# Kernel tuning notes

Measured on AMD Instinct MI355X. Metric: run time of the kernel, lower is better.

The kernel has to match this reference:

```python
import jax, jax.numpy as jnp
import numpy as np

DIM_Q = 512
DIM_K = 512
DIM_V = 512
NUM_HEADS = 8
TEMPERATURE = 0.1
LN_EPS = 1e-5


def setup_inputs() -> dict:
    key = jax.random.key(0)
    ks = jax.random.split(key, 12)
    B, n_q, n_k = 8, 1024, 1024
    s = 0.02
    return {
        "Q": jax.random.normal(ks[0], (B, n_q, DIM_Q), jnp.float32),
        "K": jax.random.normal(ks[1], (B, n_k, DIM_K), jnp.float32),
        "mask": jnp.ones((B, n_k), dtype=bool),
        "Wq": jax.random.normal(ks[2], (DIM_Q, DIM_V), jnp.float32) * s,
        "bq": jnp.zeros((DIM_V,), jnp.float32),
        "Wk": jax.random.normal(ks[3], (DIM_K, DIM_V), jnp.float32) * s,
        "bk": jnp.zeros((DIM_V,), jnp.float32),
        "Wv": jax.random.normal(ks[4], (DIM_K, DIM_V), jnp.float32) * s,
        "bv": jnp.zeros((DIM_V,), jnp.float32),
        "Wo": jax.random.normal(ks[5], (DIM_V, DIM_V), jnp.float32) * s,
        "bo": jnp.zeros((DIM_V,), jnp.float32),
        "gamma": jnp.ones((DIM_V,), jnp.float32),
        "beta": jnp.zeros((DIM_V,), jnp.float32),
    }


def _mab(Q, K, mask, Wq, bq, Wk, bk, Wv, bv, Wo, bo, gamma, beta):
    B, n_q, _ = Q.shape
    n_k = K.shape[1]
    H = NUM_HEADS
    d_head = DIM_V // H
    # projections, split heads: [B, H, n, d_head]
    Qh = (Q @ Wq + bq).reshape(B, n_q, H, d_head).transpose(0, 2, 1, 3)
    Kh = (K @ Wk + bk).reshape(B, n_k, H, d_head).transpose(0, 2, 1, 3)
    Vh = (K @ Wv + bv).reshape(B, n_k, H, d_head).transpose(0, 2, 1, 3)
    scale = 1.0 / (np.sqrt(d_head) * TEMPERATURE)
    A = jnp.einsum("bhqd,bhkd->bhqk", Qh, Kh) * scale
    A = jnp.where(mask[:, None, None, :], A, -jnp.inf)
    A = jax.nn.softmax(A, axis=-1)
    O = jnp.einsum("bhqk,bhkd->bhqd", A, Vh)
    O = O.transpose(0, 2, 1, 3).reshape(B, n_q, DIM_V)
    # fused output FFN + residual + LN
    O = O + jax.nn.relu(O @ Wo + bo)
    mu = jnp.mean(O, axis=-1, keepdims=True)
    var = jnp.var(O, axis=-1, keepdims=True)
    return (O - mu) * jax.lax.rsqrt(var + LN_EPS) * gamma + beta


def reference(Q, K, mask, Wq, bq, Wk, bk, Wv, bv, Wo, bo, gamma, beta):
    return _mab(Q, K, mask, Wq, bq, Wk, bk, Wv, bv, Wo, bo, gamma, beta)
```

## Files before the change

kernel.cpp:

```cpp
#include <hip/hip_runtime.h>

typedef __bf16 bf16;
typedef bf16 bf16x4 __attribute__((ext_vector_type(4)));
typedef bf16 bf16x8 __attribute__((ext_vector_type(8)));
typedef float floatx4 __attribute__((ext_vector_type(4)));

#define NB 8
#define NQ 1024
#define NK 1024
#define DIM 512
#define NH 8
#define DH 64

__device__ __forceinline__ void async16(const void* g, void* l) {
    __builtin_amdgcn_global_load_lds(
        (const __attribute__((address_space(1))) unsigned int*)(unsigned long long)(g),
        (__attribute__((address_space(3))) unsigned int*)(unsigned long long)(l),
        16, 0, 0);
}

__global__ __launch_bounds__(256) void prep_fused(
    const float* __restrict__ Q, const float* __restrict__ K,
    const float* __restrict__ Wq, const float* __restrict__ Wk,
    const float* __restrict__ Wv, const float* __restrict__ Wo,
    bf16* __restrict__ Qb, bf16* __restrict__ Kb, bf16* __restrict__ Wt)
{
    __shared__ bf16 Tl[64][68];
    const int bid = blockIdx.x;
    if (bid < 4096) {
        const int i = bid * 256 + threadIdx.x;
        float4 a = ((const float4*)Q)[i];
        float4 c = ((const float4*)K)[i];
        bf16x4 qa = {(bf16)a.x, (bf16)a.y, (bf16)a.z, (bf16)a.w};
        bf16x4 ka = {(bf16)c.x, (bf16)c.y, (bf16)c.z, (bf16)c.w};
        *(bf16x4*)(Qb + (size_t)i * 4) = qa;
        *(bf16x4*)(Kb + (size_t)i * 4) = ka;
    } else {
        const int bid2 = bid - 4096;
        const int w = bid2 >> 6;
        const int bx = bid2 & 7, by = (bid2 >> 3) & 7;
        const float* W = (w == 0) ? Wq : (w == 1) ? Wk : (w == 2) ? Wv : Wo;
        bf16* out = Wt + (size_t)w * DIM * DIM;
        const int k0 = bx * 64, n0 = by * 64;
        const int tx = threadIdx.x & 15, ty = threadIdx.x >> 4;
        for (int pass = 0; pass < 4; ++pass) {
            int k = ty + pass * 16;
            float4 v = *(const float4*)&W[(size_t)(k0 + k) * DIM + n0 + tx * 4];
            Tl[tx * 4 + 0][k] = (bf16)v.x;
            Tl[tx * 4 + 1][k] = (bf16)v.y;
            Tl[tx * 4 + 2][k] = (bf16)v.z;
            Tl[tx * 4 + 3][k] = (bf16)v.w;
        }
        __syncthreads();
        for (int pass = 0; pass < 4; ++pass) {
            int n = ty + pass * 16;
            bf16x4 ov = *(const bf16x4*)&Tl[n][tx * 4];
            *(bf16x4*)&out[(size_t)(n0 + n) * DIM + k0 + tx * 4] = ov;
        }
    }
}

__global__ __launch_bounds__(256) void proj_fused(
    const bf16* __restrict__ Qb, const bf16* __restrict__ Kb,
    const bf16* __restrict__ Wt,
    const float* __restrict__ bq, const float* __restrict__ bk,
    const float* __restrict__ bv,
    bf16* __restrict__ Qp, bf16* __restrict__ Kp, bf16* __restrict__ Vpt)
{
    __shared__ __attribute__((aligned(16))) bf16 sh[32768];
    const int t = threadIdx.x;
    const int wave = t >> 6, lane = t & 63, quad = lane >> 4, l16 = lane & 15;
    const int wr = wave >> 1, wc = wave & 1;
    const int bid = blockIdx.x;
    const bool isQ = bid < 256;
    const bf16* A; const bf16* W; int m0, n0;
    if (isQ) { A = Qb; W = Wt;             m0 = (bid & 63) * 128;  n0 = (bid >> 6) * 128; }
    else     { int b2 = bid - 256;
               A = Kb; W = Wt + 512 * DIM; m0 = (b2 & 63) * 128;   n0 = (b2 >> 6) * 128; }

    const int r1 = t >> 3, s1 = t & 7;
    const int p1 = s1 ^ (r1 & 7);
    const bf16* aSrc = A + (size_t)(m0 + r1) * DIM + p1 * 8;
    const bf16* wSrc = W + (size_t)(n0 + r1) * DIM + p1 * 8;

    floatx4 acc[4][4];
    for (int i = 0; i < 4; ++i)
        for (int j = 0; j < 4; ++j) acc[i][j] = (floatx4){0.f, 0.f, 0.f, 0.f};

    #pragma unroll
    for (int j = 0; j < 4; ++j) {
        async16(aSrc + (size_t)j * 32 * DIM, sh + (t + j * 256) * 8);
        async16(wSrc + (size_t)j * 32 * DIM, sh + 16384 + (t + j * 256) * 8);
    }

    for (int kt = 0; kt < 8; ++kt) {
        __syncthreads();
        const int cur = kt & 1;
        bf16* Acur = sh + cur * 8192;
        bf16* Bcur = sh + 16384 + cur * 8192;
        if (kt < 7) {
            bf16* Anxt = sh + (1 - cur) * 8192;
            bf16* Bnxt = sh + 16384 + (1 - cur) * 8192;
            const int ko = (kt + 1) * 64;
            #pragma unroll
            for (int j = 0; j < 4; ++j) {
                async16(aSrc + ko + (size_t)j * 32 * DIM, Anxt + (t + j * 256) * 8);
                async16(wSrc + ko + (size_t)j * 32 * DIM, Bnxt + (t + j * 256) * 8);
            }
        }
        #pragma unroll
        for (int ks = 0; ks < 2; ++ks) {
            bf16x8 af[4], bfr[4];
            #pragma unroll
            for (int mi = 0; mi < 4; ++mi) {
                const int row = wr * 64 + mi * 16 + l16;
                af[mi] = *(const bf16x8*)(Acur + row * 64 + (((ks * 4 + quad) ^ (row & 7)) << 3));
            }
            #pragma unroll
            for (int ni = 0; ni < 4; ++ni) {
                const int row = wc * 64 + ni * 16 + l16;
                bfr[ni] = *(const bf16x8*)(Bcur + row * 64 + (((ks * 4 + quad) ^ (row & 7)) << 3));
            }
            #pragma unroll
            for (int mi = 0; mi < 4; ++mi)
                #pragma unroll
                for (int ni = 0; ni < 4; ++ni)
                    acc[mi][ni] = __builtin_amdgcn_mfma_f32_16x16x32_bf16(
                        af[mi], bfr[ni], acc[mi][ni], 0, 0, 0);
        }
    }

    const bool isV = (!isQ) && (n0 >= 512);
    if (!isV) {
        bf16* out = isQ ? Qp : Kp;
        const float* bias = isQ ? bq : bk;
        for (int ni = 0; ni < 4; ++ni) {
            const int n = n0 + wc * 64 + ni * 16 + l16;
            const float bb = bias[n];
            const int hd = n >> 6, d = n & 63;
            for (int mi = 0; mi < 4; ++mi) {
                for (int r = 0; r < 4; ++r) {
                    const int m = m0 + wr * 64 + mi * 16 + quad * 4 + r;
                    const int b = m >> 10, q = m & 1023;
                    out[((size_t)(b * 8 + hd) * 1024 + q) * 64 + d] = (bf16)(acc[mi][ni][r] + bb);
                }
            }
        }
    } else {
        __syncthreads();
        for (int ni = 0; ni < 4; ++ni) {
            const int n = wc * 64 + ni * 16 + l16;
            const float bb = bv[n0 + n - 512];
            for (int mi = 0; mi < 4; ++mi) {
                const int mb = wr * 64 + mi * 16 + quad * 4;
                const int slot = ((mb >> 3) ^ (n & 15));
                bf16x4 pk = {(bf16)(acc[mi][ni][0] + bb), (bf16)(acc[mi][ni][1] + bb),
                             (bf16)(acc[mi][ni][2] + bb), (bf16)(acc[mi][ni][3] + bb)};
                *(bf16x4*)(sh + n * 128 + slot * 8 + (mb & 7)) = pk;
            }
        }
        __syncthreads();
        const int n = t >> 1, hf = t & 1;
        const int nv = n0 + n - 512, hd = nv >> 6, d = nv & 63;
        const int b = m0 >> 10, qb = m0 & 1023;
        bf16* dst = Vpt + ((size_t)(b * 8 + hd) * 64 + d) * 1024 + qb + hf * 64;
        #pragma unroll
        for (int j = 0; j < 8; ++j) {
            const int ch = hf * 8 + j;
            const int slot = ch ^ (n & 15);
            bf16x8 v8 = *(const bf16x8*)(sh + n * 128 + slot * 8);
            *(bf16x8*)(dst + j * 8) = v8;
        }
    }
}

__global__ __launch_bounds__(256) void attn_kernel(
    const bf16* __restrict__ Qp, const bf16* __restrict__ Kp,
    const bf16* __restrict__ Vpt, const int* __restrict__ mask,
    bf16* __restrict__ Oa)
{
    const int bh = blockIdx.x & 63, qblk = blockIdx.x >> 6;
    const int b = bh >> 3, hd = bh & 7;
    const int t = threadIdx.x;
    const int wave = t >> 6, lane = t & 63, quad = lane >> 4, l16 = lane & 15;
    const float scale = 1.25f;

    __shared__ __attribute__((aligned(16))) bf16 Kt[2][64 * 64];
    __shared__ __attribute__((aligned(16))) bf16 Vt[2][64 * 64];
    __shared__ __attribute__((aligned(16))) bf16 Pl[4][32 * 64];

    const bf16* Qbase = Qp + ((size_t)bh * NQ + qblk * 128 + wave * 32) * DH;
    const bf16* Kbase = Kp + (size_t)bh * NK * DH;
    const bf16* Vbase = Vpt + (size_t)bh * DH * NK;
    const int* mrow = mask + b * NK;

    bf16x8 qf[2][2];
    for (int g = 0; g < 2; ++g)
        for (int hh = 0; hh < 2; ++hh)
            qf[g][hh] = *(const bf16x8*)(Qbase + (g * 16 + l16) * DH + hh * 32 + quad * 8);

    floatx4 o[2][4];
    float lsum[2];
    for (int g = 0; g < 2; ++g) {
        lsum[g] = 0.f;
        for (int i = 0; i < 4; ++i) o[g][i] = (floatx4){0.f, 0.f, 0.f, 0.f};
    }

    const int r1 = t >> 3, s1 = t & 7;
    const int p1 = s1 ^ (r1 & 7);
    const bf16* kSrc = Kbase + r1 * 64 + p1 * 8;
    const bf16* vSrc = Vbase + (size_t)r1 * 1024 + p1 * 8;

    async16(kSrc, Kt[0] + t * 8);
    async16(kSrc + 32 * 64, Kt[0] + (t + 256) * 8);
    async16(vSrc, Vt[0] + t * 8);
    async16(vSrc + (size_t)32 * 1024, Vt[0] + (t + 256) * 8);

    for (int kt = 0; kt < NK / 64; ++kt) {
        __syncthreads();
        const int cur = kt & 1;
        if (kt < NK / 64 - 1) {
            const int nxt = 1 - cur;
            async16(kSrc + (kt + 1) * 4096, Kt[nxt] + t * 8);
            async16(kSrc + (kt + 1) * 4096 + 32 * 64, Kt[nxt] + (t + 256) * 8);
            async16(vSrc + (kt + 1) * 64, Vt[nxt] + t * 8);
            async16(vSrc + (kt + 1) * 64 + (size_t)32 * 1024, Vt[nxt] + (t + 256) * 8);
        }

        bf16x8 kb[4][2];
        #pragma unroll
        for (int sub = 0; sub < 4; ++sub) {
            const int rowk = sub * 16 + l16;
            kb[sub][0] = *(const bf16x8*)(Kt[cur] + rowk * 64 + ((quad ^ (rowk & 7)) << 3));
            kb[sub][1] = *(const bf16x8*)(Kt[cur] + rowk * 64 + (((quad + 4) ^ (rowk & 7)) << 3));
        }
        floatx4 sf[2][4];
        #pragma unroll
        for (int g = 0; g < 2; ++g)
            #pragma unroll
            for (int sub = 0; sub < 4; ++sub) {
                floatx4 s = {0.f, 0.f, 0.f, 0.f};
                s = __builtin_amdgcn_mfma_f32_16x16x32_bf16(kb[sub][0], qf[g][0], s, 0, 0, 0);
                s = __builtin_amdgcn_mfma_f32_16x16x32_bf16(kb[sub][1], qf[g][1], s, 0, 0, 0);
                sf[g][sub] = s;
            }
        #pragma unroll
        for (int sub = 0; sub < 4; ++sub) {
            const int4 m4 = *(const int4*)&mrow[kt * 64 + sub * 16 + quad * 4];
            const float md0 = m4.x ? 0.f : -3.0e38f;
            const float md1 = m4.y ? 0.f : -3.0e38f;
            const float md2 = m4.z ? 0.f : -3.0e38f;
            const float md3 = m4.w ? 0.f : -3.0e38f;
            #pragma unroll
            for (int g = 0; g < 2; ++g) {
                float p0 = __expf(sf[g][sub][0] * scale + md0);
                float p1v = __expf(sf[g][sub][1] * scale + md1);
                float p2 = __expf(sf[g][sub][2] * scale + md2);
                float p3 = __expf(sf[g][sub][3] * scale + md3);
                sf[g][sub][0] = p0; sf[g][sub][1] = p1v;
                sf[g][sub][2] = p2; sf[g][sub][3] = p3;
                lsum[g] += p0 + p1v + p2 + p3;
            }
        }
        #pragma unroll
        for (int g = 0; g < 2; ++g)
            #pragma unroll
            for (int sub = 0; sub < 4; ++sub) {
                bf16x4 pk = {(bf16)sf[g][sub][0], (bf16)sf[g][sub][1],
                             (bf16)sf[g][sub][2], (bf16)sf[g][sub][3]};
                const int slot = (sub * 2 + (quad >> 1)) ^ (l16 & 7);
                *(bf16x4*)&Pl[wave][(g * 16 + l16) * 64 + slot * 8 + (quad & 1) * 4] = pk;
            }
        bf16x8 af[2][2];
        #pragma unroll
        for (int g = 0; g < 2; ++g)
            #pragma unroll
            for (int hh = 0; hh < 2; ++hh) {
                const int slot = (hh * 4 + quad) ^ (l16 & 7);
                af[g][hh] = *(const bf16x8*)&Pl[wave][(g * 16 + l16) * 64 + slot * 8];
            }
        #pragma unroll
        for (int dsub = 0; dsub < 4; ++dsub) {
            const int rowd = dsub * 16 + l16;
            bf16x8 v0 = *(const bf16x8*)(Vt[cur] + rowd * 64 + ((quad ^ (rowd & 7)) << 3));
            bf16x8 v1 = *(const bf16x8*)(Vt[cur] + rowd * 64 + (((quad + 4) ^ (rowd & 7)) << 3));
            #pragma unroll
            for (int g = 0; g < 2; ++g) {
                o[g][dsub] = __builtin_amdgcn_mfma_f32_16x16x32_bf16(af[g][0], v0, o[g][dsub], 0, 0, 0);
                o[g][dsub] = __builtin_amdgcn_mfma_f32_16x16x32_bf16(af[g][1], v1, o[g][dsub], 0, 0, 0);
            }
        }
    }

    for (int g = 0; g < 2; ++g) {
        float lr = lsum[g];
        lr += __shfl_xor(lr, 16, 64);
        lr += __shfl_xor(lr, 32, 64);
        const float inv = 1.f / lr;
        float linv[4];
        for (int r = 0; r < 4; ++r) linv[r] = __shfl(inv, quad * 4 + r, 64);
        for (int dsub = 0; dsub < 4; ++dsub) {
            for (int r = 0; r < 4; ++r) {
                const int q = qblk * 128 + wave * 32 + g * 16 + quad * 4 + r;
                const int col = hd * 64 + dsub * 16 + l16;
                Oa[((size_t)(b * NQ + q)) * DIM + col] = (bf16)(o[g][dsub][r] * linv[r]);
            }
        }
    }
}

__global__ __launch_bounds__(256) void ffn_gemm(
    const bf16* __restrict__ Oa, const bf16* __restrict__ W,
    const float* __restrict__ bias, bf16* __restrict__ Yb)
{
    __shared__ __attribute__((aligned(16))) bf16 sh[32768];
    const int t = threadIdx.x;
    const int wave = t >> 6, lane = t & 63, quad = lane >> 4, l16 = lane & 15;
    const int wr = wave >> 1, wc = wave & 1;
    const int m0 = (blockIdx.x & 63) * 128, n0 = (blockIdx.x >> 6) * 128;

    const int r1 = t >> 3, s1 = t & 7;
    const int p1 = s1 ^ (r1 & 7);
    const bf16* aSrc = Oa + (size_t)(m0 + r1) * DIM + p1 * 8;
    const bf16* wSrc = W  + (size_t)(n0 + r1) * DIM + p1 * 8;

    floatx4 acc[4][4];
    for (int i = 0; i < 4; ++i)
        for (int j = 0; j < 4; ++j) acc[i][j] = (floatx4){0.f, 0.f, 0.f, 0.f};

    #pragma unroll
    for (int j = 0; j < 4; ++j) {
        async16(aSrc + (size_t)j * 32 * DIM, sh + (t + j * 256) * 8);
        async16(wSrc + (size_t)j * 32 * DIM, sh + 16384 + (t + j * 256) * 8);
    }

    for (int kt = 0; kt < 8; ++kt) {
        __syncthreads();
        const int cur = kt & 1;
        bf16* Acur = sh + cur * 8192;
        bf16* Bcur = sh + 16384 + cur * 8192;
        if (kt < 7) {
            bf16* Anxt = sh + (1 - cur) * 8192;
            bf16* Bnxt = sh + 16384 + (1 - cur) * 8192;
            const int ko = (kt + 1) * 64;
            #pragma unroll
            for (int j = 0; j < 4; ++j) {
                async16(aSrc + ko + (size_t)j * 32 * DIM, Anxt + (t + j * 256) * 8);
                async16(wSrc + ko + (size_t)j * 32 * DIM, Bnxt + (t + j * 256) * 8);
            }
        }
        #pragma unroll
        for (int ks = 0; ks < 2; ++ks) {
            bf16x8 af[4], bfr[4];
            #pragma unroll
            for (int mi = 0; mi < 4; ++mi) {
                const int row = wr * 64 + mi * 16 + l16;
                af[mi] = *(const bf16x8*)(Acur + row * 64 + (((ks * 4 + quad) ^ (row & 7)) << 3));
            }
            #pragma unroll
            for (int ni = 0; ni < 4; ++ni) {
                const int row = wc * 64 + ni * 16 + l16;
                bfr[ni] = *(const bf16x8*)(Bcur + row * 64 + (((ks * 4 + quad) ^ (row & 7)) << 3));
            }
            #pragma unroll
            for (int mi = 0; mi < 4; ++mi)
                #pragma unroll
                for (int ni = 0; ni < 4; ++ni)
                    acc[mi][ni] = __builtin_amdgcn_mfma_f32_16x16x32_bf16(
                        af[mi], bfr[ni], acc[mi][ni], 0, 0, 0);
        }
    }

    for (int ni = 0; ni < 4; ++ni) {
        const int n = n0 + wc * 64 + ni * 16 + l16;
        const float bb = bias[n];
        for (int mi = 0; mi < 4; ++mi) {
            for (int r = 0; r < 4; ++r) {
                const int m = m0 + wr * 64 + mi * 16 + quad * 4 + r;
                const float ov = (float)Oa[(size_t)m * DIM + n];
                Yb[(size_t)m * DIM + n] = (bf16)(ov + fmaxf(acc[mi][ni][r] + bb, 0.f));
            }
        }
    }
}

__global__ __launch_bounds__(256) void ln_kernel(
    const bf16* __restrict__ Y, const float* __restrict__ gamma,
    const float* __restrict__ beta, float* __restrict__ out)
{
    const int row  = blockIdx.x * 4 + (threadIdx.x >> 6);
    const int lane = threadIdx.x & 63;
    bf16x8 v = *(const bf16x8*)(Y + (size_t)row * DIM + lane * 8);
    float f[8];
    float s = 0.f, sq = 0.f;
    #pragma unroll
    for (int j = 0; j < 8; ++j) {
        f[j] = (float)v[j];
        s += f[j];
        sq += f[j] * f[j];
    }
    for (int mk = 32; mk >= 1; mk >>= 1) {
        s  += __shfl_xor(s,  mk, 64);
        sq += __shfl_xor(sq, mk, 64);
    }
    const float mu  = s * (1.f / 512.f);
    const float var = sq * (1.f / 512.f) - mu * mu;
    const float inv = rsqrtf(var + 1e-5f);
    float4 g1 = ((const float4*)gamma)[lane * 2];
    float4 g2 = ((const float4*)gamma)[lane * 2 + 1];
    float4 b1 = ((const float4*)beta)[lane * 2];
    float4 b2 = ((const float4*)beta)[lane * 2 + 1];
    float4 o1, o2;
    o1.x = (f[0] - mu) * inv * g1.x + b1.x;
    o1.y = (f[1] - mu) * inv * g1.y + b1.y;
    o1.z = (f[2] - mu) * inv * g1.z + b1.z;
    o1.w = (f[3] - mu) * inv * g1.w + b1.w;
    o2.x = (f[4] - mu) * inv * g2.x + b2.x;
    o2.y = (f[5] - mu) * inv * g2.y + b2.y;
    o2.z = (f[6] - mu) * inv * g2.z + b2.z;
    o2.w = (f[7] - mu) * inv * g2.w + b2.w;
    float* orow = out + (size_t)row * DIM;
    ((float4*)orow)[lane * 2]     = o1;
    ((float4*)orow)[lane * 2 + 1] = o2;
}

extern "C" void kernel_launch(void* const* d_in, const int* in_sizes, int n_in,
                              void* d_out, int out_size, void* d_ws, size_t ws_size,
                              hipStream_t stream) {
    const float* Q  = (const float*)d_in[0];
    const float* K  = (const float*)d_in[1];
    const int*   mask = (const int*)d_in[2];
    const float* Wq = (const float*)d_in[3];
    const float* bq = (const float*)d_in[4];
    const float* Wk = (const float*)d_in[5];
    const float* bk = (const float*)d_in[6];
    const float* Wv = (const float*)d_in[7];
    const float* bv = (const float*)d_in[8];
    const float* Wo = (const float*)d_in[9];
    const float* bo = (const float*)d_in[10];
    const float* gamma = (const float*)d_in[11];
    const float* beta  = (const float*)d_in[12];

    char* ws = (char*)d_ws;
    bf16* Wt  = (bf16*)(ws);
    bf16* Qb  = (bf16*)(ws + 2097152);
    bf16* Kb  = (bf16*)(ws + 10485760);
    bf16* Qp  = (bf16*)(ws + 18874368);
    bf16* Kp  = (bf16*)(ws + 27262976);
    bf16* Vpt = (bf16*)(ws + 35651584);
    bf16* Oa  = (bf16*)(ws + 44040192);
    bf16* Yb  = (bf16*)(ws + 52428800);
    float* out = (float*)d_out;

    prep_fused<<<4352, 256, 0, stream>>>(Q, K, Wq, Wk, Wv, Wo, Qb, Kb, Wt);
    proj_fused<<<768, 256, 0, stream>>>(Qb, Kb, Wt, bq, bk, bv, Qp, Kp, Vpt);
    attn_kernel<<<512, 256, 0, stream>>>(Qp, Kp, Vpt, mask, Oa);
    ffn_gemm<<<256, 256, 0, stream>>>(Oa, Wt + 3 * 262144, bo, Yb);
    ln_kernel<<<2048, 256, 0, stream>>>(Yb, gamma, beta, out);
}
```

Measured before the change: 177.4 us.

## Switch attention to 32x32x16 MFMA with register-resident P via permlane32 swap

Rewrites the attention inner loop to use 32x32x16 bf16 MFMAs computing S^T, so each lane owns one query row. The probabilities are repacked in registers with permlane32_swap instead of being round-tripped through shared memory, which removes the Pl buffer and its LDS traffic. Exponentials now use exp2 with a prescaled constant, and s_setprio is raised around the MFMA sections. The output store becomes vectorized bf16x4 writes, and the row-sum reduction shrinks to a single shuffle.

```diff
diff --git a/kernel.cpp b/kernel.cpp
--- a/kernel.cpp
+++ b/kernel.cpp
@@ -4,6 +4,8 @@
 typedef bf16 bf16x4 __attribute__((ext_vector_type(4)));
 typedef bf16 bf16x8 __attribute__((ext_vector_type(8)));
 typedef float floatx4 __attribute__((ext_vector_type(4)));
+typedef float floatx16 __attribute__((ext_vector_type(16)));
+typedef unsigned int uintx2 __attribute__((ext_vector_type(2)));
 
 #define NB 8
 #define NQ 1024
@@ -182,29 +184,29 @@
     const int bh = blockIdx.x & 63, qblk = blockIdx.x >> 6;
     const int b = bh >> 3, hd = bh & 7;
     const int t = threadIdx.x;
-    const int wave = t >> 6, lane = t & 63, quad = lane >> 4, l16 = lane & 15;
-    const float scale = 1.25f;
+    const int wave = t >> 6, lane = t & 63;
+    const int l31 = lane & 31, hi = lane >> 5;
+    const float SC = 1.8033688f;
 
     __shared__ __attribute__((aligned(16))) bf16 Kt[2][64 * 64];
     __shared__ __attribute__((aligned(16))) bf16 Vt[2][64 * 64];
-    __shared__ __attribute__((aligned(16))) bf16 Pl[4][32 * 64];
 
     const bf16* Qbase = Qp + ((size_t)bh * NQ + qblk * 128 + wave * 32) * DH;
     const bf16* Kbase = Kp + (size_t)bh * NK * DH;
     const bf16* Vbase = Vpt + (size_t)bh * DH * NK;
     const int* mrow = mask + b * NK;
 
-    bf16x8 qf[2][2];
-    for (int g = 0; g < 2; ++g)
-        for (int hh = 0; hh < 2; ++hh)
-            qf[g][hh] = *(const bf16x8*)(Qbase + (g * 16 + l16) * DH + hh * 32 + quad * 8);
-
-    floatx4 o[2][4];
-    float lsum[2];
-    for (int g = 0; g < 2; ++g) {
-        lsum[g] = 0.f;
-        for (int i = 0; i < 4; ++i) o[g][i] = (floatx4){0.f, 0.f, 0.f, 0.f};
-    }
+    bf16x8 qf[4];
+    #pragma unroll
+    for (int st = 0; st < 4; ++st)
+        qf[st] = *(const bf16x8*)(Qbase + (size_t)l31 * DH + st * 16 + hi * 8);
+
+    floatx16 o[2];
+    #pragma unroll
+    for (int d = 0; d < 2; ++d)
+        #pragma unroll
+        for (int i = 0; i < 16; ++i) o[d][i] = 0.f;
+    float lsum = 0.f;
 
     const int r1 = t >> 3, s1 = t & 7;
     const int p1 = s1 ^ (r1 & 7);
@@ -227,86 +229,81 @@
             async16(vSrc + (kt + 1) * 64 + (size_t)32 * 1024, Vt[nxt] + (t + 256) * 8);
         }
 
-        bf16x8 kb[4][2];
-        #pragma unroll
-        for (int sub = 0; sub < 4; ++sub) {
-            const int rowk = sub * 16 + l16;
-            kb[sub][0] = *(const bf16x8*)(Kt[cur] + rowk * 64 + ((quad ^ (rowk & 7)) << 3));
-            kb[sub][1] = *(const bf16x8*)(Kt[cur] + rowk * 64 + (((quad + 4) ^ (rowk & 7)) << 3));
-        }
-        floatx4 sf[2][4];
-        #pragma unroll
-        for (int g = 0; g < 2; ++g)
-            #pragma unroll
-            for (int sub = 0; sub < 4; ++sub) {
-                floatx4 s = {0.f, 0.f, 0.f, 0.f};
-                s = __builtin_amdgcn_mfma_f32_16x16x32_bf16(kb[sub][0], qf[g][0], s, 0, 0, 0);
-                s = __builtin_amdgcn_mfma_f32_16x16x32_bf16(kb[sub][1], qf[g][1], s, 0, 0, 0);
-                sf[g][sub] = s;
-            }
-        #pragma unroll
-        for (int sub = 0; sub < 4; ++sub) {
-            const int4 m4 = *(const int4*)&mrow[kt * 64 + sub * 16 + quad * 4];
-            const float md0 = m4.x ? 0.f : -3.0e38f;
-            const float md1 = m4.y ? 0.f : -3.0e38f;
-            const float md2 = m4.z ? 0.f : -3.0e38f;
-            const float md3 = m4.w ? 0.f : -3.0e38f;
-            #pragma unroll
-            for (int g = 0; g < 2; ++g) {
-                float p0 = __expf(sf[g][sub][0] * scale + md0);
-                float p1v = __expf(sf[g][sub][1] * scale + md1);
-                float p2 = __expf(sf[g][sub][2] * scale + md2);
-                float p3 = __expf(sf[g][sub][3] * scale + md3);
-                sf[g][sub][0] = p0; sf[g][sub][1] = p1v;
-                sf[g][sub][2] = p2; sf[g][sub][3] = p3;
-                lsum[g] += p0 + p1v + p2 + p3;
-            }
-        }
-        #pragma unroll
-        for (int g = 0; g < 2; ++g)
-            #pragma unroll
-            for (int sub = 0; sub < 4; ++sub) {
-                bf16x4 pk = {(bf16)sf[g][sub][0], (bf16)sf[g][sub][1],
-                             (bf16)sf[g][sub][2], (bf16)sf[g][sub][3]};
-                const int slot = (sub * 2 + (quad >> 1)) ^ (l16 & 7);
-                *(bf16x4*)&Pl[wave][(g * 16 + l16) * 64 + slot * 8 + (quad & 1) * 4] = pk;
-            }
-        bf16x8 af[2][2];
-        #pragma unroll
-        for (int g = 0; g < 2; ++g)
-            #pragma unroll
-            for (int hh = 0; hh < 2; ++hh) {
-                const int slot = (hh * 4 + quad) ^ (l16 & 7);
-                af[g][hh] = *(const bf16x8*)&Pl[wave][(g * 16 + l16) * 64 + slot * 8];
-            }
-        #pragma unroll
-        for (int dsub = 0; dsub < 4; ++dsub) {
-            const int rowd = dsub * 16 + l16;
-            bf16x8 v0 = *(const bf16x8*)(Vt[cur] + rowd * 64 + ((quad ^ (rowd & 7)) << 3));
-            bf16x8 v1 = *(const bf16x8*)(Vt[cur] + rowd * 64 + (((quad + 4) ^ (rowd & 7)) << 3));
-            #pragma unroll
-            for (int g = 0; g < 2; ++g) {
-                o[g][dsub] = __builtin_amdgcn_mfma_f32_16x16x32_bf16(af[g][0], v0, o[g][dsub], 0, 0, 0);
-                o[g][dsub] = __builtin_amdgcn_mfma_f32_16x16x32_bf16(af[g][1], v1, o[g][dsub], 0, 0, 0);
-            }
-        }
-    }
-
-    for (int g = 0; g < 2; ++g) {
-        float lr = lsum[g];
-        lr += __shfl_xor(lr, 16, 64);
-        lr += __shfl_xor(lr, 32, 64);
-        const float inv = 1.f / lr;
-        float linv[4];
-        for (int r = 0; r < 4; ++r) linv[r] = __shfl(inv, quad * 4 + r, 64);
-        for (int dsub = 0; dsub < 4; ++dsub) {
-            for (int r = 0; r < 4; ++r) {
-                const int q = qblk * 128 + wave * 32 + g * 16 + quad * 4 + r;
-                const int col = hd * 64 + dsub * 16 + l16;
-                Oa[((size_t)(b * NQ + q)) * DIM + col] = (bf16)(o[g][dsub][r] * linv[r]);
-            }
-        }
-    }
+        floatx16 sf[2];
+        __builtin_amdgcn_s_setprio(1);
+        #pragma unroll
+        for (int sub = 0; sub < 2; ++sub) {
+            floatx16 s;
+            #pragma unroll
+            for (int i = 0; i < 16; ++i) s[i] = 0.f;
+            const int row = sub * 32 + l31;
+            #pragma unroll
+            for (int st = 0; st < 4; ++st) {
+                bf16x8 ka = *(const bf16x8*)(Kt[cur] + row * 64 +
+                                             (((st * 2 + hi) ^ (row & 7)) << 3));
+                s = __builtin_amdgcn_mfma_f32_32x32x16_bf16(ka, qf[st], s, 0, 0, 0);
+            }
+            sf[sub] = s;
+        }
+        __builtin_amdgcn_s_setprio(0);
+
+        unsigned int w[2][4][2];
+        #pragma unroll
+        for (int sub = 0; sub < 2; ++sub)
+            #pragma unroll
+            for (int m = 0; m < 4; ++m) {
+                const int4 m4 = *(const int4*)&mrow[kt * 64 + sub * 32 + m * 8 + hi * 4];
+                const float md0 = m4.x ? 0.f : -1.0e38f;
+                const float md1 = m4.y ? 0.f : -1.0e38f;
+                const float md2 = m4.z ? 0.f : -1.0e38f;
+                const float md3 = m4.w ? 0.f : -1.0e38f;
+                const float p0 = __builtin_amdgcn_exp2f(sf[sub][m * 4 + 0] * SC + md0);
+                const float p1 = __builtin_amdgcn_exp2f(sf[sub][m * 4 + 1] * SC + md1);
+                const float p2 = __builtin_amdgcn_exp2f(sf[sub][m * 4 + 2] * SC + md2);
+                const float p3 = __builtin_amdgcn_exp2f(sf[sub][m * 4 + 3] * SC + md3);
+                lsum += (p0 + p1) + (p2 + p3);
+                union { bf16 h[2]; unsigned int u; } pkA, pkB;
+                pkA.h[0] = (bf16)p0; pkA.h[1] = (bf16)p1;
+                pkB.h[0] = (bf16)p2; pkB.h[1] = (bf16)p3;
+                w[sub][m][0] = pkA.u;
+                w[sub][m][1] = pkB.u;
+            }
+
+        __builtin_amdgcn_s_setprio(1);
+        #pragma unroll
+        for (int sub = 0; sub < 2; ++sub)
+            #pragma unroll
+            for (int ks = 0; ks < 2; ++ks) {
+                uintx2 e0 = __builtin_amdgcn_permlane32_swap(
+                    w[sub][2 * ks + 0][0], w[sub][2 * ks + 1][0], false, false);
+                uintx2 e1 = __builtin_amdgcn_permlane32_swap(
+                    w[sub][2 * ks + 0][1], w[sub][2 * ks + 1][1], false, false);
+                union { unsigned int u[4]; bf16x8 v; } pb;
+                pb.u[0] = e0[0]; pb.u[1] = e1[0]; pb.u[2] = e0[1]; pb.u[3] = e1[1];
+                const int kc = sub * 2 + ks;
+                #pragma unroll
+                for (int dsub = 0; dsub < 2; ++dsub) {
+                    const int row = dsub * 32 + l31;
+                    bf16x8 va = *(const bf16x8*)(Vt[cur] + row * 64 +
+                                                 (((kc * 2 + hi) ^ (row & 7)) << 3));
+                    o[dsub] = __builtin_amdgcn_mfma_f32_32x32x16_bf16(va, pb.v, o[dsub], 0, 0, 0);
+                }
+            }
+        __builtin_amdgcn_s_setprio(0);
+    }
+
+    lsum += __shfl_xor(lsum, 32, 64);
+    const float inv = 1.f / lsum;
+    const int q = qblk * 128 + wave * 32 + l31;
+    bf16* orow = Oa + ((size_t)(b * NQ + q)) * DIM + hd * 64;
+    #pragma unroll
+    for (int dsub = 0; dsub < 2; ++dsub)
+        #pragma unroll
+        for (int rg = 0; rg < 4; ++rg) {
+            bf16x4 st = {(bf16)(o[dsub][rg * 4 + 0] * inv), (bf16)(o[dsub][rg * 4 + 1] * inv),
+                         (bf16)(o[dsub][rg * 4 + 2] * inv), (bf16)(o[dsub][rg * 4 + 3] * inv)};
+            *(bf16x4*)(orow + dsub * 32 + rg * 8 + hi * 4) = st;
+        }
 }
 
 __global__ __launch_bounds__(256) void ffn_gemm(
```

Result: no change. 176.5 us (-0.5%).

## Halve attention query tile per block, use exp2 and MFMA priority hints

Applied to the files above, without the earlier changes.

The attention kernel now gives each wave 16 query rows instead of 32, so each block covers 64 queries and the grid doubles to 1024 blocks. The aim is more parallelism and occupancy on the many CUs, at the cost of reloading K/V tiles twice as often per query. The exp is replaced with the hardware exp2 using a prefolded log2e scale. MFMA sections are wrapped in s_setprio to favour matrix issue.

```diff
diff --git a/kernel.cpp b/kernel.cpp
--- a/kernel.cpp
+++ b/kernel.cpp
@@ -183,28 +183,26 @@
     const int b = bh >> 3, hd = bh & 7;
     const int t = threadIdx.x;
     const int wave = t >> 6, lane = t & 63, quad = lane >> 4, l16 = lane & 15;
-    const float scale = 1.25f;
+    const float SC = 1.8033688f;
 
     __shared__ __attribute__((aligned(16))) bf16 Kt[2][64 * 64];
     __shared__ __attribute__((aligned(16))) bf16 Vt[2][64 * 64];
-    __shared__ __attribute__((aligned(16))) bf16 Pl[4][32 * 64];
-
-    const bf16* Qbase = Qp + ((size_t)bh * NQ + qblk * 128 + wave * 32) * DH;
+    __shared__ __attribute__((aligned(16))) bf16 Pl[4][16 * 64];
+
+    const bf16* Qbase = Qp + ((size_t)bh * NQ + qblk * 64 + wave * 16) * DH;
     const bf16* Kbase = Kp + (size_t)bh * NK * DH;
     const bf16* Vbase = Vpt + (size_t)bh * DH * NK;
     const int* mrow = mask + b * NK;
 
-    bf16x8 qf[2][2];
-    for (int g = 0; g < 2; ++g)
-        for (int hh = 0; hh < 2; ++hh)
-            qf[g][hh] = *(const bf16x8*)(Qbase + (g * 16 + l16) * DH + hh * 32 + quad * 8);
-
-    floatx4 o[2][4];
-    float lsum[2];
-    for (int g = 0; g < 2; ++g) {
-        lsum[g] = 0.f;
-        for (int i = 0; i < 4; ++i) o[g][i] = (floatx4){0.f, 0.f, 0.f, 0.f};
-    }
+    bf16x8 qf[2];
+    #pragma unroll
+    for (int hh = 0; hh < 2; ++hh)
+        qf[hh] = *(const bf16x8*)(Qbase + (size_t)l16 * DH + hh * 32 + quad * 8);
+
+    floatx4 o[4];
+    float lsum = 0.f;
+    #pragma unroll
+    for (int i = 0; i < 4; ++i) o[i] = (floatx4){0.f, 0.f, 0.f, 0.f};
 
     const int r1 = t >> 3, s1 = t & 7;
     const int p1 = s1 ^ (r1 & 7);
@@ -234,16 +232,16 @@
             kb[sub][0] = *(const bf16x8*)(Kt[cur] + rowk * 64 + ((quad ^ (rowk & 7)) << 3));
             kb[sub][1] = *(const bf16x8*)(Kt[cur] + rowk * 64 + (((quad + 4) ^ (rowk & 7)) << 3));
         }
-        floatx4 sf[2][4];
-        #pragma unroll
-        for (int g = 0; g < 2; ++g)
-            #pragma unroll
-            for (int sub = 0; sub < 4; ++sub) {
-                floatx4 s = {0.f, 0.f, 0.f, 0.f};
-                s = __builtin_amdgcn_mfma_f32_16x16x32_bf16(kb[sub][0], qf[g][0], s, 0, 0, 0);
-                s = __builtin_amdgcn_mfma_f32_16x16x32_bf16(kb[sub][1], qf[g][1], s, 0, 0, 0);
-                sf[g][sub] = s;
-            }
+        floatx4 sf[4];
+        __builtin_amdgcn_s_setprio(1);
+        #pragma unroll
+        for (int sub = 0; sub < 4; ++sub) {
+            floatx4 s = {0.f, 0.f, 0.f, 0.f};
+            s = __builtin_amdgcn_mfma_f32_16x16x32_bf16(kb[sub][0], qf[0], s, 0, 0, 0);
+            s = __builtin_amdgcn_mfma_f32_16x16x32_bf16(kb[sub][1], qf[1], s, 0, 0, 0);
+            sf[sub] = s;
+        }
+        __builtin_amdgcn_s_setprio(0);
         #pragma unroll
         for (int sub = 0; sub < 4; ++sub) {
             const int4 m4 = *(const int4*)&mrow[kt * 64 + sub * 16 + quad * 4];
@@ -251,60 +249,50 @@
             const float md1 = m4.y ? 0.f : -3.0e38f;
             const float md2 = m4.z ? 0.f : -3.0e38f;
             const float md3 = m4.w ? 0.f : -3.0e38f;
-            #pragma unroll
-            for (int g = 0; g < 2; ++g) {
-                float p0 = __expf(sf[g][sub][0] * scale + md0);
-                float p1v = __expf(sf[g][sub][1] * scale + md1);
-                float p2 = __expf(sf[g][sub][2] * scale + md2);
-                float p3 = __expf(sf[g][sub][3] * scale + md3);
-                sf[g][sub][0] = p0; sf[g][sub][1] = p1v;
-                sf[g][sub][2] = p2; sf[g][sub][3] = p3;
-                lsum[g] += p0 + p1v + p2 + p3;
-            }
-        }
-        #pragma unroll
-        for (int g = 0; g < 2; ++g)
-            #pragma unroll
-            for (int sub = 0; sub < 4; ++sub) {
-                bf16x4 pk = {(bf16)sf[g][sub][0], (bf16)sf[g][sub][1],
-                             (bf16)sf[g][sub][2], (bf16)sf[g][sub][3]};
-                const int slot = (sub * 2 + (quad >> 1)) ^ (l16 & 7);
-                *(bf16x4*)&Pl[wave][(g * 16 + l16) * 64 + slot * 8 + (quad & 1) * 4] = pk;
-            }
-        bf16x8 af[2][2];
-        #pragma unroll
-        for (int g = 0; g < 2; ++g)
-            #pragma unroll
-            for (int hh = 0; hh < 2; ++hh) {
-                const int slot = (hh * 4 + quad) ^ (l16 & 7);
-                af[g][hh] = *(const bf16x8*)&Pl[wave][(g * 16 + l16) * 64 + slot * 8];
-            }
+            const float p0 = __builtin_amdgcn_exp2f(sf[sub][0] * SC + md0);
+            const float p1 = __builtin_amdgcn_exp2f(sf[sub][1] * SC + md1);
+            const float p2 = __builtin_amdgcn_exp2f(sf[sub][2] * SC + md2);
+            const float p3 = __builtin_amdgcn_exp2f(sf[sub][3] * SC + md3);
+            sf[sub][0] = p0; sf[sub][1] = p1; sf[sub][2] = p2; sf[sub][3] = p3;
+            lsum += (p0 + p1) + (p2 + p3);
+        }
+        #pragma unroll
+        for (int sub = 0; sub < 4; ++sub) {
+            bf16x4 pk = {(bf16)sf[sub][0], (bf16)sf[sub][1],
+                         (bf16)sf[sub][2], (bf16)sf[sub][3]};
+            const int slot = (sub * 2 + (quad >> 1)) ^ (l16 & 7);
+            *(bf16x4*)&Pl[wave][l16 * 64 + slot * 8 + (quad & 1) * 4] = pk;
+        }
+        bf16x8 af[2];
+        #pragma unroll
+        for (int hh = 0; hh < 2; ++hh) {
+            const int slot = (hh * 4 + quad) ^ (l16 & 7);
+            af[hh] = *(const bf16x8*)&Pl[wave][l16 * 64 + slot * 8];
+        }
+        __builtin_amdgcn_s_setprio(1);
         #pragma unroll
         for (int dsub = 0; dsub < 4; ++dsub) {
             const int rowd = dsub * 16 + l16;
             bf16x8 v0 = *(const bf16x8*)(Vt[cur] + rowd * 64 + ((quad ^ (rowd & 7)) << 3));
             bf16x8 v1 = *(const bf16x8*)(Vt[cur] + rowd * 64 + (((quad + 4) ^ (rowd & 7)) << 3));
-            #pragma unroll
-            for (int g = 0; g < 2; ++g) {
-                o[g][dsub] = __builtin_amdgcn_mfma_f32_16x16x32_bf16(af[g][0], v0, o[g][dsub], 0, 0, 0);
-                o[g][dsub] = __builtin_amdgcn_mfma_f32_16x16x32_bf16(af[g][1], v1, o[g][dsub], 0, 0, 0);
-            }
-        }
-    }
-
-    for (int g = 0; g < 2; ++g) {
-        float lr = lsum[g];
-        lr += __shfl_xor(lr, 16, 64);
-        lr += __shfl_xor(lr, 32, 64);
-        const float inv = 1.f / lr;
-        float linv[4];
-        for (int r = 0; r < 4; ++r) linv[r] = __shfl(inv, quad * 4 + r, 64);
-        for (int dsub = 0; dsub < 4; ++dsub) {
-            for (int r = 0; r < 4; ++r) {
-                const int q = qblk * 128 + wave * 32 + g * 16 + quad * 4 + r;
-                const int col = hd * 64 + dsub * 16 + l16;
-                Oa[((size_t)(b * NQ + q)) * DIM + col] = (bf16)(o[g][dsub][r] * linv[r]);
-            }
+            o[dsub] = __builtin_amdgcn_mfma_f32_16x16x32_bf16(af[0], v0, o[dsub], 0, 0, 0);
+            o[dsub] = __builtin_amdgcn_mfma_f32_16x16x32_bf16(af[1], v1, o[dsub], 0, 0, 0);
+        }
+        __builtin_amdgcn_s_setprio(0);
+    }
+
+    float lr = lsum;
+    lr += __shfl_xor(lr, 16, 64);
+    lr += __shfl_xor(lr, 32, 64);
+    const float inv = 1.f / lr;
+    float linv[4];
+    #pragma unroll
+    for (int r = 0; r < 4; ++r) linv[r] = __shfl(inv, quad * 4 + r, 64);
+    for (int dsub = 0; dsub < 4; ++dsub) {
+        for (int r = 0; r < 4; ++r) {
+            const int q = qblk * 64 + wave * 16 + quad * 4 + r;
+            const int col = hd * 64 + dsub * 16 + l16;
+            Oa[((size_t)(b * NQ + q)) * DIM + col] = (bf16)(o[dsub][r] * linv[r]);
         }
     }
 }
@@ -454,7 +442,7 @@
 
     prep_fused<<<4352, 256, 0, stream>>>(Q, K, Wq, Wk, Wv, Wo, Qb, Kb, Wt);
     proj_fused<<<768, 256, 0, stream>>>(Qb, Kb, Wt, bq, bk, bv, Qp, Kp, Vpt);
-    attn_kernel<<<512, 256, 0, stream>>>(Qp, Kp, Vpt, mask, Oa);
+    attn_kernel<<<1024, 256, 0, stream>>>(Qp, Kp, Vpt, mask, Oa);
     ffn_gemm<<<256, 256, 0, stream>>>(Oa, Wt + 3 * 262144, bo, Yb);
     ln_kernel<<<2048, 256, 0, stream>>>(Yb, gamma, beta, out);
 }
```

New measurement: 170.4 us. 1.04x faster.
